# Kernel tuning notes

Measured on AMD Instinct MI355X. Metric: run time of the kernel, lower is better.

Reference implementation:

```python
import jax, jax.numpy as jnp
import numpy as np

BT, N = 4, 2048
FIN, FOUT = 512, 128          # GGE in/out; FOUT == PPI output (GAGA constraint)
PIN, POUT = 256, 128          # PPIGE in/out
HEAD = 4
K = POUT // HEAD              # per-head dim = 32
NEG_SLOPE = 0.2
MASK_VAL = -1e30


def setup_inputs() -> dict:
    key = jax.random.key(0)
    ks = jax.random.split(key, 24)
    s = 0.05
    inp = {}
    inp["a"] = jax.random.normal(ks[0], (BT, FIN), jnp.float32)
    inp["bio_a"] = jax.random.normal(ks[1], (BT, N, PIN), jnp.float32)
    inp["A"] = jax.random.randint(ks[2], (BT, N, N), 0, 2, jnp.int32)
    inp["b"] = jax.random.normal(ks[3], (BT, FIN), jnp.float32)
    inp["bio_b"] = jax.random.normal(ks[4], (BT, N, PIN), jnp.float32)
    inp["B"] = jax.random.randint(ks[5], (BT, N, N), 0, 2, jnp.int32)
    # PPIGE_GAT params (shared across both graph branches)
    inp["initW"] = jax.random.normal(ks[6], (POUT, PIN), jnp.float32) * s
    inp["initb"] = jnp.zeros((POUT,), jnp.float32)
    inp["projW"] = jax.random.normal(ks[7], (POUT, POUT), jnp.float32) * s  # no bias
    inp["attw"] = jax.random.normal(ks[8], (HEAD, 2 * K), jnp.float32) * s  # per-head [2k]->1
    inp["attb"] = jnp.zeros((HEAD,), jnp.float32)
    # GGE params
    inp["ggeW1"] = jax.random.normal(ks[9], (128, FIN), jnp.float32) * s
    inp["ggeb1"] = jnp.zeros((128,), jnp.float32)
    inp["ggeW2"] = jax.random.normal(ks[10], (FOUT, 128), jnp.float32) * s
    inp["ggeb2"] = jnp.zeros((FOUT,), jnp.float32)
    # LED params (hidden = FOUT)
    inp["convW"] = jax.random.normal(ks[11], (2 * FOUT, 2 * FOUT), jnp.float32) * s  # k=1 conv
    inp["convb"] = jnp.zeros((2 * FOUT,), jnp.float32)
    inp["ledW1"] = jax.random.normal(ks[12], (FOUT, 4 * FOUT), jnp.float32) * s
    inp["ledb1"] = jnp.zeros((FOUT,), jnp.float32)
    inp["ledW2"] = jax.random.normal(ks[13], (2, FOUT), jnp.float32) * s
    inp["ledb2"] = jnp.zeros((2,), jnp.float32)
    return inp


def _gat_layer(x, adj_mask, projW, attw, attb):
    # x: [B,N,POUT]; adj_mask: [B,N,N] bool
    Bt, n, _ = x.shape
    xh = (x @ projW.T).reshape(Bt, n, HEAD, K).transpose(0, 2, 1, 3)  # [B,h,N,k]
    # score(i,j) = leaky_relu(w1.x_i + w2.x_j + b)  (equivalent to Linear on concat)
    s1 = jnp.einsum('bhnk,hk->bhn', xh, attw[:, :K])
    s2 = jnp.einsum('bhnk,hk->bhn', xh, attw[:, K:])
    scores = jax.nn.leaky_relu(
        s1[..., :, None] + s2[..., None, :] + attb[None, :, None, None], NEG_SLOPE)
    scores = jnp.where(adj_mask[:, None], scores, MASK_VAL)
    att = jax.nn.softmax(scores, axis=-1)                     # [B,h,N,N]
    out = jax.nn.relu(att @ xh)                               # [B,h,N,k]
    return out.transpose(0, 2, 1, 3).reshape(Bt, n, HEAD * K)


def _ppige(bio, adj, initW, initb, projW, attw, attb):
    x = bio @ initW.T + initb
    return _gat_layer(x, adj > 0, projW, attw, attb) + x      # residual; dropout=eval


def _gge(a, W1, b1, W2, b2):
    h = jax.nn.relu(a @ W1.T + b1)
    return jax.nn.relu(h @ W2.T + b2)


def _gaga(G, h):
    # G: [B,N,D], h: [B,D]
    att = jax.nn.softmax(jnp.einsum('bnd,bd->bn', G, h), axis=-1)
    return jnp.einsum('bnd,bn->bd', G, att)


def _led(ea, eb, convW, convb, W1, b1, W2, b2):
    # pointwise conv over the length-2 stack [ea, eb], then maxpool over length
    cnn = jnp.maximum(ea @ convW.T + convb, eb @ convW.T + convb)  # [B,2D]
    x = jax.nn.relu(jnp.concatenate([cnn, ea - eb], axis=1) @ W1.T + b1)
    return x @ W2.T + b2


def reference(a, bio_a, A, b, bio_b, B,
              initW, initb, projW, attw, attb,
              ggeW1, ggeb1, ggeW2, ggeb2,
              convW, convb, ledW1, ledb1, ledW2, ledb2):
    G_a = _ppige(bio_a, A, initW, initb, projW, attw, attb)
    G_b = _ppige(bio_b, B, initW, initb, projW, attw, attb)
    h_a = _gge(a, ggeW1, ggeb1, ggeW2, ggeb2)
    h_b = _gge(b, ggeW1, ggeb1, ggeW2, ggeb2)
    e_a = jnp.concatenate([h_a, _gaga(G_a, h_a)], axis=-1)
    e_b = jnp.concatenate([h_b, _gaga(G_b, h_b)], axis=-1)
    logits = _led(e_a, e_b, convW, convb, ledW1, ledb1, ledW2, ledb2)
    return jax.nn.log_softmax(logits, axis=-1)
```

## Files before the change

kernel.cpp:

```cpp
#include <hip/hip_runtime.h>
#include <hip/hip_bf16.h>
#include <math.h>

#define NN 2048
#define NEG 0.2f
#define LOG2E 1.44269504f

typedef short bf16x8 __attribute__((ext_vector_type(8)));
typedef float f32x16 __attribute__((ext_vector_type(16)));

__device__ __forceinline__ float dot4(float4 a, float4 b) {
  return a.x * b.x + a.y * b.y + a.z * b.z + a.w * b.w;
}

__device__ __forceinline__ unsigned short bfbits(float f) {
  union { __hip_bfloat16 b; unsigned short u; } c;
  c.b = __float2bfloat16(f);
  return c.u;
}

__global__ __launch_bounds__(256) void k1_init(const float* __restrict__ bioA,
                                               const float* __restrict__ bioB,
                                               const float* __restrict__ W,
                                               const float* __restrict__ bias,
                                               float* __restrict__ xout) {
  __shared__ float As[32][36];
  __shared__ float Ws[32][132];
  const int t = threadIdx.x;
  const int m0 = blockIdx.x * 32;
  const float* A = (m0 < 8192) ? bioA : bioB;
  const int arow0 = (m0 < 8192) ? m0 : (m0 - 8192);
  const int og = t & 31, ig = t >> 5;
  float acc[4][4] = {};
  for (int kt = 0; kt < 256; kt += 32) {
    __syncthreads();
    {
      const int r = t >> 3, kq = t & 7;
      const float4 v = *(const float4*)&A[(arow0 + r) * 256 + kt + kq * 4];
      As[kq * 4 + 0][r] = v.x; As[kq * 4 + 1][r] = v.y;
      As[kq * 4 + 2][r] = v.z; As[kq * 4 + 3][r] = v.w;
    }
#pragma unroll
    for (int u = 0; u < 4; ++u) {
      const int f = u * 256 + t;
      const int o = f >> 3, kq = f & 7;
      const float4 v = *(const float4*)&W[o * 256 + kt + kq * 4];
      Ws[kq * 4 + 0][o] = v.x; Ws[kq * 4 + 1][o] = v.y;
      Ws[kq * 4 + 2][o] = v.z; Ws[kq * 4 + 3][o] = v.w;
    }
    __syncthreads();
#pragma unroll
    for (int kk = 0; kk < 32; ++kk) {
      const float4 a4 = *(const float4*)&As[kk][ig * 4];
      const float4 w4 = *(const float4*)&Ws[kk][og * 4];
      const float av[4] = {a4.x, a4.y, a4.z, a4.w};
      const float wv[4] = {w4.x, w4.y, w4.z, w4.w};
#pragma unroll
      for (int ii = 0; ii < 4; ++ii)
#pragma unroll
        for (int jj = 0; jj < 4; ++jj) acc[ii][jj] += av[ii] * wv[jj];
    }
  }
  const float4 b4 = *(const float4*)&bias[og * 4];
#pragma unroll
  for (int ii = 0; ii < 4; ++ii) {
    const int row = m0 + ig * 4 + ii;
    float4 o4;
    o4.x = acc[ii][0] + b4.x; o4.y = acc[ii][1] + b4.y;
    o4.z = acc[ii][2] + b4.z; o4.w = acc[ii][3] + b4.w;
    *(float4*)&xout[row * 128 + og * 4] = o4;
  }
}

__global__ __launch_bounds__(256) void k2_proj(const float* __restrict__ x,
                                               const float* __restrict__ W,
                                               const float* __restrict__ attw,
                                               unsigned short* __restrict__ xhT2,
                                               float* __restrict__ s1,
                                               float* __restrict__ s2) {
  __shared__ float As[32][36];
  __shared__ float Ws[32][132];
  const int t = threadIdx.x;
  const int m0 = blockIdx.x * 32;
  const int og = t & 31, ig = t >> 5;
  float acc[4][4] = {};
  for (int kt = 0; kt < 128; kt += 32) {
    __syncthreads();
    {
      const int r = t >> 3, kq = t & 7;
      const float4 v = *(const float4*)&x[(m0 + r) * 128 + kt + kq * 4];
      As[kq * 4 + 0][r] = v.x; As[kq * 4 + 1][r] = v.y;
      As[kq * 4 + 2][r] = v.z; As[kq * 4 + 3][r] = v.w;
    }
#pragma unroll
    for (int u = 0; u < 4; ++u) {
      const int f = u * 256 + t;
      const int o = f >> 3, kq = f & 7;
      const float4 v = *(const float4*)&W[o * 128 + kt + kq * 4];
      Ws[kq * 4 + 0][o] = v.x; Ws[kq * 4 + 1][o] = v.y;
      Ws[kq * 4 + 2][o] = v.z; Ws[kq * 4 + 3][o] = v.w;
    }
    __syncthreads();
#pragma unroll
    for (int kk = 0; kk < 32; ++kk) {
      const float4 a4 = *(const float4*)&As[kk][ig * 4];
      const float4 w4 = *(const float4*)&Ws[kk][og * 4];
      const float av[4] = {a4.x, a4.y, a4.z, a4.w};
      const float wv[4] = {w4.x, w4.y, w4.z, w4.w};
#pragma unroll
      for (int ii = 0; ii < 4; ++ii)
#pragma unroll
        for (int jj = 0; jj < 4; ++jj) acc[ii][jj] += av[ii] * wv[jj];
    }
  }
  const int h = og >> 3;
  const int k4i = (og & 7) * 4;
  const int g = m0 >> 13;
  const int bb = (m0 >> 11) & 3;
  const int gb = g * 4 + bb;
  const int n0 = (m0 & 2047) + ig * 4;
  const float4 w1 = *(const float4*)&attw[h * 64 + k4i];
  const float4 w2 = *(const float4*)&attw[h * 64 + 32 + k4i];
  float p1[4], p2[4];
#pragma unroll
  for (int ii = 0; ii < 4; ++ii) {
    float4 v;
    v.x = acc[ii][0]; v.y = acc[ii][1]; v.z = acc[ii][2]; v.w = acc[ii][3];
    p1[ii] = dot4(v, w1);
    p2[ii] = dot4(v, w2);
  }
  {
    const int mtile = n0 >> 4, jslot = (n0 >> 3) & 1, j8 = n0 & 7;
    const int base2 = ((((gb * 4 + h) * 128 + mtile) * 2 + jslot) * 32) * 8 + j8;
#pragma unroll
    for (int jj = 0; jj < 4; ++jj) {
      const int kin = k4i + jj;
      ushort4 u;
      u.x = bfbits(acc[0][jj]); u.y = bfbits(acc[1][jj]);
      u.z = bfbits(acc[2][jj]); u.w = bfbits(acc[3][jj]);
      *(ushort4*)&xhT2[base2 + kin * 8] = u;
    }
  }
#pragma unroll
  for (int s = 1; s < 8; s <<= 1) {
#pragma unroll
    for (int ii = 0; ii < 4; ++ii) {
      p1[ii] += __shfl_xor(p1[ii], s);
      p2[ii] += __shfl_xor(p2[ii], s);
    }
  }
  if ((og & 7) == 0) {
#pragma unroll
    for (int ii = 0; ii < 4; ++ii) {
      s1[(gb * 4 + h) * NN + n0 + ii] = p1[ii];
      s2[(gb * 4 + h) * NN + n0 + ii] = p2[ii];
    }
  }
}

#define K3_PROLOGUE                                                           \
  {                                                                           \
    const float* s2g = s2w + gb * 4 * NN;                                     \
    _Pragma("unroll")                                                         \
    for (int u = 0; u < 4; ++u) {                                             \
      const int idx = u * 2048 + t * 4;                                       \
      float4 v = *(const float4*)&s2g[idx];                                   \
      v.x *= LOG2E; v.y *= LOG2E; v.z *= LOG2E; v.w *= LOG2E;                 \
      *(float4*)&s2L[idx] = v;                                                \
    }                                                                         \
  }                                                                           \
  _Pragma("unroll")                                                           \
  for (int r4 = 0; r4 < 4; ++r4) {                                            \
    const int r = wave * 4 + r4;                                              \
    const int* arow = adj + r * NN;                                           \
    int av[32];                                                               \
    _Pragma("unroll")                                                         \
    for (int w = 0; w < 32; ++w) av[w] = arow[w * 64 + lane];                 \
    _Pragma("unroll")                                                         \
    for (int w = 0; w < 32; ++w) {                                            \
      const unsigned long long mm = __ballot(av[w] > 0);                      \
      if (lane < 2) adjL[r * 66 + 2 * w + lane] = (unsigned int)(mm >> (32 * lane)); \
    }                                                                         \
  }

#define K3_SCORE_BODY(MM)                                                     \
    const int j0 = jlo + 16 * (MM) + jslot * 8;                               \
    const unsigned int wbits = adjL[i * 66 + ((jlo + 16 * (MM)) >> 5)];       \
    const unsigned int bits8 = wbits >> ((((MM) & 1) * 16) + jslot * 8);      \
    const float4 s2a = *(const float4*)&s2L[h * 2048 + j0];                   \
    const float4 s2b = *(const float4*)&s2L[h * 2048 + j0 + 4];               \
    const float sv[8] = {s2a.x, s2a.y, s2a.z, s2a.w,                          \
                         s2b.x, s2b.y, s2b.z, s2b.w};                         \
    union { bf16x8 v; unsigned short u[8]; } af;                              \
    float dsum = 0.f;                                                         \
    _Pragma("unroll")                                                         \
    for (int e = 0; e < 8; ++e) {                                             \
      float s = sc1v + sv[e];                                                 \
      s = fmaxf(s, NEG * s);                                                  \
      float pe = __builtin_amdgcn_exp2f(s);                                   \
      pe = ((bits8 >> e) & 1u) ? pe : 0.f;                                    \
      af.u[e] = bfbits(pe);                                                   \
      dsum += pe;                                                             \
    }                                                                         \
    den += dsum;

__global__ __launch_bounds__(512) void k3_attn(const unsigned short* __restrict__ xhT2,
                                               const float* __restrict__ s1w,
                                               const float* __restrict__ s2w,
                                               const int* __restrict__ adjA,
                                               const int* __restrict__ adjB,
                                               const float* __restrict__ attb,
                                               const float* __restrict__ x,
                                               float* __restrict__ G) {
  __shared__ __align__(16) unsigned char smem3[42240];
  unsigned int* adjL = (unsigned int*)smem3;
  float* s2L = (float*)(smem3 + 8448);
  float* denR = (float*)(smem3 + 41216);
  float* accR = (float*)smem3;

  const int t = threadIdx.x;
  const int wave = t >> 6, lane = t & 63;
  const int blk = blockIdx.x;
  const int g = blk >> 8, b = (blk >> 6) & 3;
  const int i0 = (blk & 63) * 32;
  const int gb = g * 4 + b;
  const int* adj = (g ? adjB : adjA) + (b * NN + i0) * NN;
  K3_PROLOGUE
  __syncthreads();

  const int h = wave & 3;
  const int jhalf = wave >> 2;
  const int jlo = jhalf * 1024;
  const int i = lane & 31;
  const int jslot = lane >> 5;
  const float sc1v = (s1w[(gb * 4 + h) * NN + i0 + i] + attb[h]) * LOG2E;
  const unsigned short* bbase = xhT2 + (gb * 4 + h) * 65536 + jhalf * 32768 + lane * 8;
  f32x16 acc = {0.f, 0.f, 0.f, 0.f, 0.f, 0.f, 0.f, 0.f,
                0.f, 0.f, 0.f, 0.f, 0.f, 0.f, 0.f, 0.f};
  float den = 0.f;

#define K3_CSTEP(RB, MM)                                                      \
  {                                                                           \
    K3_SCORE_BODY(MM)                                                         \
    acc = __builtin_amdgcn_mfma_f32_32x32x16_bf16(af.v, RB, acc, 0, 0, 0);    \
  }

  bf16x8 ba0 = *(const bf16x8*)&bbase[0 * 512];
  bf16x8 ba1 = *(const bf16x8*)&bbase[1 * 512];
  bf16x8 ba2 = *(const bf16x8*)&bbase[2 * 512];
  bf16x8 ba3 = *(const bf16x8*)&bbase[3 * 512];
  __builtin_amdgcn_sched_barrier(0);
  for (int mb = 0; mb < 64; mb += 8) {
    bf16x8 bb0 = *(const bf16x8*)&bbase[(mb + 4) * 512];
    bf16x8 bb1 = *(const bf16x8*)&bbase[(mb + 5) * 512];
    bf16x8 bb2 = *(const bf16x8*)&bbase[(mb + 6) * 512];
    bf16x8 bb3 = *(const bf16x8*)&bbase[(mb + 7) * 512];
    __builtin_amdgcn_sched_barrier(0);
    K3_CSTEP(ba0, mb + 0)
    K3_CSTEP(ba1, mb + 1)
    K3_CSTEP(ba2, mb + 2)
    K3_CSTEP(ba3, mb + 3)
    __builtin_amdgcn_sched_barrier(0);
    if (mb < 56) {
      ba0 = *(const bf16x8*)&bbase[(mb + 8) * 512];
      ba1 = *(const bf16x8*)&bbase[(mb + 9) * 512];
      ba2 = *(const bf16x8*)&bbase[(mb + 10) * 512];
      ba3 = *(const bf16x8*)&bbase[(mb + 11) * 512];
    }
    __builtin_amdgcn_sched_barrier(0);
    K3_CSTEP(bb0, mb + 4)
    K3_CSTEP(bb1, mb + 5)
    K3_CSTEP(bb2, mb + 6)
    K3_CSTEP(bb3, mb + 7)
    __builtin_amdgcn_sched_barrier(0);
  }
#undef K3_CSTEP

  den += __shfl_xor(den, 32);
  if (lane < 32) denR[(h * 2 + jhalf) * 32 + lane] = den;
  __syncthreads();
  if (jhalf == 1) {
#pragma unroll
    for (int r = 0; r < 16; ++r) accR[(h * 16 + r) * 65 + lane] = acc[r];
  }
  __syncthreads();
  if (jhalf == 0) {
#pragma unroll
    for (int r = 0; r < 16; ++r) {
      const int row = (r & 3) + 8 * (r >> 2) + 4 * jslot;
      const float dinv = 1.f / (denR[(h * 2 + 0) * 32 + row] + denR[(h * 2 + 1) * 32 + row]);
      const int off = (gb * NN + i0 + row) * 128 + h * 32 + i;
      const float av2 = acc[r] + accR[(h * 16 + r) * 65 + lane];
      G[off] = fmaxf(av2 * dinv, 0.f) + x[off];
    }
  }
}

__global__ __launch_bounds__(256) void k4h_gge(const float* __restrict__ a_in,
                                               const float* __restrict__ b_in,
                                               const float* __restrict__ ggeW1,
                                               const float* __restrict__ ggeb1,
                                               const float* __restrict__ ggeW2,
                                               const float* __restrict__ ggeb2,
                                               float* __restrict__ hvbuf,
                                               float* __restrict__ e) {
  __shared__ float inL[512];
  __shared__ float h1L[128];
  const int t = threadIdx.x;
  const int wave = t >> 6, lane = t & 63;
  const int g = blockIdx.x >> 2, b = blockIdx.x & 3;
  const int gb2 = g * 4 + b;
  const float* inp = (g ? b_in : a_in) + b * 512;
  if (t < 128) *(float4*)&inL[t * 4] = *(const float4*)&inp[t * 4];
  __syncthreads();
  for (int p = 0; p < 16; ++p) {
    const int o0 = p * 8 + wave * 2;
    const float* w0 = &ggeW1[o0 * 512 + lane * 8];
    const float* w1 = &ggeW1[(o0 + 1) * 512 + lane * 8];
    const float4 i0v = *(const float4*)&inL[lane * 8];
    const float4 i1v = *(const float4*)&inL[lane * 8 + 4];
    float s0 = dot4(*(const float4*)&w0[0], i0v) + dot4(*(const float4*)&w0[4], i1v);
    float s1v = dot4(*(const float4*)&w1[0], i0v) + dot4(*(const float4*)&w1[4], i1v);
#pragma unroll
    for (int s = 1; s < 64; s <<= 1) { s0 += __shfl_xor(s0, s); s1v += __shfl_xor(s1v, s); }
    if (lane == 0) {
      h1L[o0] = fmaxf(s0 + ggeb1[o0], 0.f);
      h1L[o0 + 1] = fmaxf(s1v + ggeb1[o0 + 1], 0.f);
    }
  }
  __syncthreads();
  for (int p = 0; p < 16; ++p) {
    const int o0 = p * 8 + wave * 2;
    const float2 w0 = *(const float2*)&ggeW2[o0 * 128 + lane * 2];
    const float2 w1 = *(const float2*)&ggeW2[(o0 + 1) * 128 + lane * 2];
    const float2 hvv = *(const float2*)&h1L[lane * 2];
    float s0 = w0.x * hvv.x + w0.y * hvv.y;
    float s1v = w1.x * hvv.x + w1.y * hvv.y;
#pragma unroll
    for (int s = 1; s < 64; s <<= 1) { s0 += __shfl_xor(s0, s); s1v += __shfl_xor(s1v, s); }
    if (lane == 0) {
      const float v0 = fmaxf(s0 + ggeb2[o0], 0.f);
      const float v1 = fmaxf(s1v + ggeb2[o0 + 1], 0.f);
      hvbuf[gb2 * 128 + o0] = v0;
      hvbuf[gb2 * 128 + o0 + 1] = v1;
      e[gb2 * 256 + o0] = v0;
      e[gb2 * 256 + o0 + 1] = v1;
    }
  }
}

__global__ __launch_bounds__(256) void k4a_logits(const float* __restrict__ G,
                                                  const float* __restrict__ hv,
                                                  float* __restrict__ lg) {
  const int t = threadIdx.x;
  const int wave = t >> 6, lane = t & 63;
  const int gb = blockIdx.x >> 4, chunk = blockIdx.x & 15;
  const float2 hvv = *(const float2*)&hv[gb * 128 + lane * 2];
  const float* Gb = G + gb * NN * 128;
  const int nbase = chunk * 128 + wave * 32;
  for (int q = 0; q < 32; ++q) {
    const int n = nbase + q;
    const float2 gv = *(const float2*)&Gb[n * 128 + lane * 2];
    float part = gv.x * hvv.x + gv.y * hvv.y;
#pragma unroll
    for (int s = 1; s < 64; s <<= 1) part += __shfl_xor(part, s);
    if (lane == 0) lg[gb * NN + n] = part;
  }
}

__global__ __launch_bounds__(256) void k4b_reduce(const float* __restrict__ lg,
                                                  float* __restrict__ mz) {
  __shared__ float red[256];
  const int t = threadIdx.x;
  const int gb = blockIdx.x;
  const float* l = lg + gb * NN;
  float m = -1e30f;
  for (int n = t; n < NN; n += 256) m = fmaxf(m, l[n]);
  red[t] = m; __syncthreads();
#pragma unroll
  for (int s = 128; s > 0; s >>= 1) {
    if (t < s) red[t] = fmaxf(red[t], red[t + s]);
    __syncthreads();
  }
  const float mx = red[0]; __syncthreads();
  float z = 0.f;
  for (int n = t; n < NN; n += 256) z += __expf(l[n] - mx);
  red[t] = z; __syncthreads();
#pragma unroll
  for (int s = 128; s > 0; s >>= 1) {
    if (t < s) red[t] += red[t + s];
    __syncthreads();
  }
  if (t == 0) { mz[gb * 2] = mx; mz[gb * 2 + 1] = red[0]; }
}

__global__ __launch_bounds__(256) void k4c_wsum(const float* __restrict__ G,
                                                const float* __restrict__ lg,
                                                const float* __restrict__ mz,
                                                float* __restrict__ wsum) {
  __shared__ float pL[128];
  __shared__ float red[2][128];
  const int t = threadIdx.x;
  const int gb = blockIdx.x >> 4, chunk = blockIdx.x & 15;
  const float mx = mz[gb * 2];
  if (t < 128) pL[t] = __expf(lg[gb * NN + chunk * 128 + t] - mx);
  __syncthreads();
  const int d = t & 127, half = t >> 7;
  const float* Gb = G + (gb * NN + chunk * 128 + half * 64) * 128;
  float acc = 0.f;
  for (int q = 0; q < 64; ++q) acc += pL[half * 64 + q] * Gb[q * 128 + d];
  red[half][d] = acc;
  __syncthreads();
  if (t < 128) wsum[(gb * 16 + chunk) * 128 + t] = red[0][t] + red[1][t];
}

__global__ __launch_bounds__(128) void k4d_final(const float* __restrict__ wsum,
                                                 const float* __restrict__ mz,
                                                 float* __restrict__ e) {
  const int t = threadIdx.x;
  const int gb = blockIdx.x;
  float s = 0.f;
#pragma unroll
  for (int c = 0; c < 16; ++c) s += wsum[(gb * 16 + c) * 128 + t];
  e[gb * 256 + 128 + t] = s / mz[gb * 2 + 1];
}

__global__ __launch_bounds__(256) void k5_led(const float* __restrict__ e,
                                              const float* __restrict__ convW,
                                              const float* __restrict__ convb,
                                              const float* __restrict__ ledW1,
                                              const float* __restrict__ ledb1,
                                              const float* __restrict__ ledW2,
                                              const float* __restrict__ ledb2,
                                              float* __restrict__ out) {
  __shared__ float eaL[256], ebL[256], uL[512], xL[128], lgL[2];
  const int t = threadIdx.x;
  const int wave = t >> 6, lane = t & 63;
  const int bt = blockIdx.x;
  if (t < 64) {
    *(float4*)&eaL[t * 4] = *(const float4*)&e[bt * 256 + t * 4];
    *(float4*)&ebL[t * 4] = *(const float4*)&e[(4 + bt) * 256 + t * 4];
  }
  __syncthreads();
  uL[256 + t] = eaL[t] - ebL[t];
  const float4 ea4 = *(const float4*)&eaL[lane * 4];
  const float4 eb4 = *(const float4*)&ebL[lane * 4];
  for (int p = 0; p < 32; ++p) {
    const int o0 = p * 8 + wave * 2;
    const float4 w0 = *(const float4*)&convW[o0 * 256 + lane * 4];
    const float4 w1 = *(const float4*)&convW[(o0 + 1) * 256 + lane * 4];
    float sa0 = dot4(w0, ea4), sb0 = dot4(w0, eb4);
    float sa1 = dot4(w1, ea4), sb1 = dot4(w1, eb4);
#pragma unroll
    for (int s = 1; s < 64; s <<= 1) {
      sa0 += __shfl_xor(sa0, s); sb0 += __shfl_xor(sb0, s);
      sa1 += __shfl_xor(sa1, s); sb1 += __shfl_xor(sb1, s);
    }
    if (lane == 0) {
      const float c0 = convb[o0], c1 = convb[o0 + 1];
      uL[o0] = fmaxf(sa0 + c0, sb0 + c0);
      uL[o0 + 1] = fmaxf(sa1 + c1, sb1 + c1);
    }
  }
  __syncthreads();
  for (int p = 0; p < 16; ++p) {
    const int o0 = p * 8 + wave * 2;
    const float* w0 = &ledW1[o0 * 512 + lane * 8];
    const float* w1 = &ledW1[(o0 + 1) * 512 + lane * 8];
    const float4 u0 = *(const float4*)&uL[lane * 8];
    const float4 u1 = *(const float4*)&uL[lane * 8 + 4];
    float s0 = dot4(*(const float4*)&w0[0], u0) + dot4(*(const float4*)&w0[4], u1);
    float s1v = dot4(*(const float4*)&w1[0], u0) + dot4(*(const float4*)&w1[4], u1);
#pragma unroll
    for (int s = 1; s < 64; s <<= 1) { s0 += __shfl_xor(s0, s); s1v += __shfl_xor(s1v, s); }
    if (lane == 0) {
      xL[o0] = fmaxf(s0 + ledb1[o0], 0.f);
      xL[o0 + 1] = fmaxf(s1v + ledb1[o0 + 1], 0.f);
    }
  }
  __syncthreads();
  if (wave < 2) {
    const float2 w = *(const float2*)&ledW2[wave * 128 + lane * 2];
    const float2 xv = *(const float2*)&xL[lane * 2];
    float s0 = w.x * xv.x + w.y * xv.y;
#pragma unroll
    for (int s = 1; s < 64; s <<= 1) s0 += __shfl_xor(s0, s);
    if (lane == 0) lgL[wave] = s0 + ledb2[wave];
  }
  __syncthreads();
  if (t == 0) {
    const float l0 = lgL[0], l1 = lgL[1];
    const float m = fmaxf(l0, l1);
    const float za = __expf(l0 - m) + __expf(l1 - m);
    const float lz = __logf(za);
    out[bt * 2 + 0] = l0 - m - lz;
    out[bt * 2 + 1] = l1 - m - lz;
  }
}

extern "C" void kernel_launch(void* const* d_in, const int* in_sizes, int n_in,
                              void* d_out, int out_size, void* d_ws, size_t ws_size,
                              hipStream_t stream) {
  (void)in_sizes; (void)n_in; (void)out_size; (void)ws_size;
  const float* a     = (const float*)d_in[0];
  const float* bioA  = (const float*)d_in[1];
  const int*   A     = (const int*)d_in[2];
  const float* b     = (const float*)d_in[3];
  const float* bioB  = (const float*)d_in[4];
  const int*   B     = (const int*)d_in[5];
  const float* initW = (const float*)d_in[6];
  const float* initb = (const float*)d_in[7];
  const float* projW = (const float*)d_in[8];
  const float* attw  = (const float*)d_in[9];
  const float* attb  = (const float*)d_in[10];
  const float* ggeW1 = (const float*)d_in[11];
  const float* ggeb1 = (const float*)d_in[12];
  const float* ggeW2 = (const float*)d_in[13];
  const float* ggeb2 = (const float*)d_in[14];
  const float* convW = (const float*)d_in[15];
  const float* convb = (const float*)d_in[16];
  const float* ledW1 = (const float*)d_in[17];
  const float* ledb1 = (const float*)d_in[18];
  const float* ledW2 = (const float*)d_in[19];
  const float* ledb2 = (const float*)d_in[20];

  float* ws = (float*)d_ws;
  float*          x    = ws;
  unsigned short* xhT2 = (unsigned short*)(ws + 2097152);
  float*          s1   = ws + 3145728;
  float*          s2   = ws + 3211264;
  float*          G    = ws + 3276800;
  float*          lg   = ws + 5373952;
  float*          wsum = ws + 5390336;
  float*          mz   = ws + 5406720;
  float*          hv   = ws + 5406736;
  float*          e    = ws + 5407760;
  float* out = (float*)d_out;

  k1_init<<<512, 256, 0, stream>>>(bioA, bioB, initW, initb, x);
  k2_proj<<<512, 256, 0, stream>>>(x, projW, attw, xhT2, s1, s2);
  k3_attn<<<512, 512, 0, stream>>>(xhT2, s1, s2, A, B, attb, x, G);
  k4h_gge<<<8, 256, 0, stream>>>(a, b, ggeW1, ggeb1, ggeW2, ggeb2, hv, e);
  k4a_logits<<<128, 256, 0, stream>>>(G, hv, lg);
  k4b_reduce<<<8, 256, 0, stream>>>(lg, mz);
  k4c_wsum<<<128, 256, 0, stream>>>(G, lg, mz, wsum);
  k4d_final<<<8, 128, 0, stream>>>(wsum, mz, e);
  k5_led<<<4, 256, 0, stream>>>(e, convW, convb, ledW1, ledb1, ledW2, ledb2, out);
}
```

Baseline: 178.2 us.

## Deepen B-operand prefetch, remap block order, and stream adjacency nontemporally

The attention kernel now keeps sixteen bf16 B-fragments in flight in four rotating groups instead of two groups of four, so global load latency is hidden further ahead of the MFMA chain. The block index is also permuted so that consecutive launched blocks land on different graph/batch slices, which spreads memory traffic across channels and L2. Adjacency rows are read once, so they now use nontemporal loads to avoid polluting the cache. In exchange the kernel holds more live VGPRs, which may reduce occupancy.

```diff
diff --git a/kernel.cpp b/kernel.cpp
--- a/kernel.cpp
+++ b/kernel.cpp
@@ -175,7 +175,7 @@
     const int* arow = adj + r * NN;                                           \
     int av[32];                                                               \
     _Pragma("unroll")                                                         \
-    for (int w = 0; w < 32; ++w) av[w] = arow[w * 64 + lane];                 \
+    for (int w = 0; w < 32; ++w) av[w] = __builtin_nontemporal_load(&arow[w * 64 + lane]); \
     _Pragma("unroll")                                                         \
     for (int w = 0; w < 32; ++w) {                                            \
       const unsigned long long mm = __ballot(av[w] > 0);                      \
@@ -220,7 +220,8 @@
 
   const int t = threadIdx.x;
   const int wave = t >> 6, lane = t & 63;
-  const int blk = blockIdx.x;
+  const int p = (int)blockIdx.x;
+  const int blk = (p & 7) * 64 + (p >> 3);
   const int g = blk >> 8, b = (blk >> 6) & 3;
   const int i0 = (blk & 63) * 32;
   const int gb = g * 4 + b;
@@ -245,33 +246,71 @@
     acc = __builtin_amdgcn_mfma_f32_32x32x16_bf16(af.v, RB, acc, 0, 0, 0);    \
   }
 
-  bf16x8 ba0 = *(const bf16x8*)&bbase[0 * 512];
-  bf16x8 ba1 = *(const bf16x8*)&bbase[1 * 512];
-  bf16x8 ba2 = *(const bf16x8*)&bbase[2 * 512];
-  bf16x8 ba3 = *(const bf16x8*)&bbase[3 * 512];
+  bf16x8 fa0 = *(const bf16x8*)&bbase[0 * 512];
+  bf16x8 fa1 = *(const bf16x8*)&bbase[1 * 512];
+  bf16x8 fa2 = *(const bf16x8*)&bbase[2 * 512];
+  bf16x8 fa3 = *(const bf16x8*)&bbase[3 * 512];
+  bf16x8 fb0 = *(const bf16x8*)&bbase[4 * 512];
+  bf16x8 fb1 = *(const bf16x8*)&bbase[5 * 512];
+  bf16x8 fb2 = *(const bf16x8*)&bbase[6 * 512];
+  bf16x8 fb3 = *(const bf16x8*)&bbase[7 * 512];
+  bf16x8 fc0 = *(const bf16x8*)&bbase[8 * 512];
+  bf16x8 fc1 = *(const bf16x8*)&bbase[9 * 512];
+  bf16x8 fc2 = *(const bf16x8*)&bbase[10 * 512];
+  bf16x8 fc3 = *(const bf16x8*)&bbase[11 * 512];
+  bf16x8 fd0 = *(const bf16x8*)&bbase[12 * 512];
+  bf16x8 fd1 = *(const bf16x8*)&bbase[13 * 512];
+  bf16x8 fd2 = *(const bf16x8*)&bbase[14 * 512];
+  bf16x8 fd3 = *(const bf16x8*)&bbase[15 * 512];
   __builtin_amdgcn_sched_barrier(0);
-  for (int mb = 0; mb < 64; mb += 8) {
-    bf16x8 bb0 = *(const bf16x8*)&bbase[(mb + 4) * 512];
-    bf16x8 bb1 = *(const bf16x8*)&bbase[(mb + 5) * 512];
-    bf16x8 bb2 = *(const bf16x8*)&bbase[(mb + 6) * 512];
-    bf16x8 bb3 = *(const bf16x8*)&bbase[(mb + 7) * 512];
-    __builtin_amdgcn_sched_barrier(0);
-    K3_CSTEP(ba0, mb + 0)
-    K3_CSTEP(ba1, mb + 1)
-    K3_CSTEP(ba2, mb + 2)
-    K3_CSTEP(ba3, mb + 3)
-    __builtin_amdgcn_sched_barrier(0);
-    if (mb < 56) {
-      ba0 = *(const bf16x8*)&bbase[(mb + 8) * 512];
-      ba1 = *(const bf16x8*)&bbase[(mb + 9) * 512];
-      ba2 = *(const bf16x8*)&bbase[(mb + 10) * 512];
-      ba3 = *(const bf16x8*)&bbase[(mb + 11) * 512];
-    }
-    __builtin_amdgcn_sched_barrier(0);
-    K3_CSTEP(bb0, mb + 4)
-    K3_CSTEP(bb1, mb + 5)
-    K3_CSTEP(bb2, mb + 6)
-    K3_CSTEP(bb3, mb + 7)
+  for (int mb = 0; mb < 64; mb += 16) {
+    K3_CSTEP(fa0, mb + 0)
+    K3_CSTEP(fa1, mb + 1)
+    K3_CSTEP(fa2, mb + 2)
+    K3_CSTEP(fa3, mb + 3)
+    __builtin_amdgcn_sched_barrier(0);
+    if (mb < 48) {
+      fa0 = *(const bf16x8*)&bbase[(mb + 16) * 512];
+      fa1 = *(const bf16x8*)&bbase[(mb + 17) * 512];
+      fa2 = *(const bf16x8*)&bbase[(mb + 18) * 512];
+      fa3 = *(const bf16x8*)&bbase[(mb + 19) * 512];
+    }
+    __builtin_amdgcn_sched_barrier(0);
+    K3_CSTEP(fb0, mb + 4)
+    K3_CSTEP(fb1, mb + 5)
+    K3_CSTEP(fb2, mb + 6)
+    K3_CSTEP(fb3, mb + 7)
+    __builtin_amdgcn_sched_barrier(0);
+    if (mb < 48) {
+      fb0 = *(const bf16x8*)&bbase[(mb + 20) * 512];
+      fb1 = *(const bf16x8*)&bbase[(mb + 21) * 512];
+      fb2 = *(const bf16x8*)&bbase[(mb + 22) * 512];
+      fb3 = *(const bf16x8*)&bbase[(mb + 23) * 512];
+    }
+    __builtin_amdgcn_sched_barrier(0);
+    K3_CSTEP(fc0, mb + 8)
+    K3_CSTEP(fc1, mb + 9)
+    K3_CSTEP(fc2, mb + 10)
+    K3_CSTEP(fc3, mb + 11)
+    __builtin_amdgcn_sched_barrier(0);
+    if (mb < 48) {
+      fc0 = *(const bf16x8*)&bbase[(mb + 24) * 512];
+      fc1 = *(const bf16x8*)&bbase[(mb + 25) * 512];
+      fc2 = *(const bf16x8*)&bbase[(mb + 26) * 512];
+      fc3 = *(const bf16x8*)&bbase[(mb + 27) * 512];
+    }
+    __builtin_amdgcn_sched_barrier(0);
+    K3_CSTEP(fd0, mb + 12)
+    K3_CSTEP(fd1, mb + 13)
+    K3_CSTEP(fd2, mb + 14)
+    K3_CSTEP(fd3, mb + 15)
+    __builtin_amdgcn_sched_barrier(0);
+    if (mb < 48) {
+      fd0 = *(const bf16x8*)&bbase[(mb + 28) * 512];
+      fd1 = *(const bf16x8*)&bbase[(mb + 29) * 512];
+      fd2 = *(const bf16x8*)&bbase[(mb + 30) * 512];
+      fd3 = *(const bf16x8*)&bbase[(mb + 31) * 512];
+    }
     __builtin_amdgcn_sched_barrier(0);
   }
 #undef K3_CSTEP
```

Result: slower. 187.5 us (+5.2%).
